# Kernel optimization log

Hardware: AMD Instinct MI355X
Metric: run time of the kernel (lower is better)

The kernel has to match this reference:

```python
import jax, jax.numpy as jnp
import numpy as np

D_MODEL = 1024
N_HEADS = 16
D_K = D_MODEL // N_HEADS
B, S = 4, 2048


def setup_inputs() -> dict:
    key = jax.random.key(0)
    ks = jax.random.split(key, 9)
    sc = 1.0 / np.sqrt(D_MODEL)
    inp = {
        "x": jax.random.normal(ks[0], (B, S, D_MODEL), dtype=jnp.float32),
        # causal mask, broadcastable over batch and heads; 0 -> masked
        "mask": jnp.tril(jnp.ones((S, S), dtype=jnp.int32))[None, None, :, :],
        "Wq": jax.random.normal(ks[1], (D_MODEL, D_MODEL), dtype=jnp.float32) * sc,
        "bq": jax.random.normal(ks[2], (D_MODEL,), dtype=jnp.float32) * sc,
        "Wk": jax.random.normal(ks[3], (D_MODEL, D_MODEL), dtype=jnp.float32) * sc,
        "bk": jax.random.normal(ks[4], (D_MODEL,), dtype=jnp.float32) * sc,
        "Wv": jax.random.normal(ks[5], (D_MODEL, D_MODEL), dtype=jnp.float32) * sc,
        "bv": jax.random.normal(ks[6], (D_MODEL,), dtype=jnp.float32) * sc,
        "Wo": jax.random.normal(ks[7], (D_MODEL, D_MODEL), dtype=jnp.float32) * sc,
        "bo": jax.random.normal(ks[8], (D_MODEL,), dtype=jnp.float32) * sc,
    }
    return inp


def _split_heads(t):
    b, s, _ = t.shape
    return t.reshape(b, s, N_HEADS, D_K).transpose(0, 2, 1, 3)  # [B,H,S,dk]


def reference(x, mask, Wq, bq, Wk, bk, Wv, bv, Wo, bo):
    Q = _split_heads(x @ Wq.T + bq)
    K = _split_heads(x @ Wk.T + bk)
    V = _split_heads(x @ Wv.T + bv)
    scores = jnp.einsum("bhqd,bhkd->bhqk", Q, K) / jnp.sqrt(jnp.float32(D_K))
    scores = jnp.where(mask == 0, jnp.float32(-1e9), scores)
    weights = jax.nn.softmax(scores, axis=-1)
    attn = jnp.einsum("bhqk,bhkd->bhqd", weights, V)  # [B,H,S,dk]
    attn = attn.transpose(0, 2, 1, 3).reshape(x.shape[0], x.shape[1], D_MODEL)
    return attn @ Wo.T + bo
```

## Files before the change

kernel.cpp:

```cpp
#include <hip/hip_runtime.h>
#include <hip/hip_bf16.h>
#include <cstdint>

#define DM   1024
#define NH   16
#define DK   64
#define BB   4
#define SS   2048
#define MTOT (BB * SS)
#define PAD  68

typedef short short8 __attribute__((ext_vector_type(8)));
typedef float f32x4  __attribute__((ext_vector_type(4)));
using u16 = unsigned short;

__device__ inline u16 f2b(float f) {
    union { float f; unsigned int u; } v; v.f = f;
    unsigned int u = v.u;
    u += 0x7fffu + ((u >> 16) & 1u);
    return (u16)(u >> 16);
}
__device__ inline u16 f2b_trunc(float f) {
    union { float f; unsigned int u; } v; v.f = f;
    return (u16)(v.u >> 16);
}
__device__ inline float b2f(u16 s) {
    union { unsigned int u; float f; } v; v.u = ((unsigned int)s) << 16;
    return v.f;
}

__device__ inline void load_lds16(const u16* g, u16* l) {
    __builtin_amdgcn_global_load_lds(
        (const __attribute__((address_space(1))) unsigned int*)g,
        (__attribute__((address_space(3))) unsigned int*)l, 16, 0, 0);
}

struct CvtPtrs {
    const void *x, *Wq, *Wk, *Wv, *Wo, *bq, *bk, *bv, *bo;
    u16 *xb, *Wqb, *Wkb, *Wvb, *Wob, *bqb, *bkb, *bvb, *bob;
};

__global__ void convert_all(CvtPtrs p, int* __restrict__ flag)
{
    __shared__ int cnt;
    if (threadIdx.x == 0) cnt = 0;
    __syncthreads();
    int c = 0;
    for (int i = threadIdx.x; i < 512; i += 256) {
        const int e = (((const u16*)p.x)[i] >> 7) & 0xFF;
        if (e >= 100 && e <= 140) c++;
    }
    atomicAdd(&cnt, c);
    __syncthreads();
    const int isbf = (cnt >= 420) ? 1 : 0;
    if (blockIdx.x == 0 && threadIdx.x == 0) *flag = isbf;
    if (isbf) return;

    const size_t E  = (size_t)MTOT * DM;
    const size_t W1 = (size_t)DM * DM;
    const size_t i = ((size_t)blockIdx.x * blockDim.x + threadIdx.x) * 8;
    const float* s; u16* d; size_t off;
    if (i < E) {
        s = (const float*)p.x; d = p.xb; off = i;
    } else {
        size_t j = i - E;
        if (j < (W1 << 2)) {
            const int w = (int)(j >> 20); off = j & (W1 - 1);
            const float* ss[4] = {(const float*)p.Wq, (const float*)p.Wk,
                                  (const float*)p.Wv, (const float*)p.Wo};
            u16* dd[4] = {p.Wqb, p.Wkb, p.Wvb, p.Wob};
            s = ss[w]; d = dd[w];
        } else {
            j -= (W1 << 2);
            if (j >= 4 * DM) return;
            const int w = (int)(j >> 10); off = j & (DM - 1);
            const float* ss[4] = {(const float*)p.bq, (const float*)p.bk,
                                  (const float*)p.bv, (const float*)p.bo};
            u16* dd[4] = {p.bqb, p.bkb, p.bvb, p.bob};
            s = ss[w]; d = dd[w];
        }
    }
    const float4 f0 = *(const float4*)(s + off);
    const float4 f1 = *(const float4*)(s + off + 4);
    u16 tmp[8] = {f2b(f0.x), f2b(f0.y), f2b(f0.z), f2b(f0.w),
                  f2b(f1.x), f2b(f1.y), f2b(f1.z), f2b(f1.w)};
    *(int4*)(d + off) = *(const int4*)tmp;
}

__device__ __forceinline__
void gemm_body(const u16* __restrict__ A, const u16* __restrict__ Bw,
               const u16* __restrict__ bias, void* __restrict__ out,
               int mode, float scale, int isbf, int m0, int n0,
               u16 (*As)[64], u16 (*Bs)[64])
{
    const int tid  = threadIdx.x;
    const int wave = tid >> 6;
    const int lane = tid & 63;
    const int wm = (wave >> 1) * 64;
    const int wn = (wave & 1) * 64;

    const int lm   = lane & 15;
    const int quad = lane >> 4;
    const int kq   = quad * 8;
    const int rq   = quad * 4;

    const int lrow   = lane >> 3;
    const int lchunk = (lane & 7) ^ lrow;
    const u16* gA = A  + (size_t)(m0 + 8*wave + lrow) * DM + lchunk * 8;
    const u16* gB = Bw + (size_t)(n0 + 8*wave + lrow) * DM + lchunk * 8;
    u16* ldsA = (u16*)((char*)&As[0][0] + wave * 1024);
    u16* ldsB = (u16*)((char*)&Bs[0][0] + wave * 1024);

    f32x4 acc[4][4] = {};

    for (int k0 = 0; k0 < DM; k0 += 64) {
        __syncthreads();
#pragma unroll
        for (int c = 0; c < 4; c++) {
            load_lds16(gA + (size_t)c*32*DM + k0, (u16*)((char*)ldsA + c*4096));
            load_lds16(gB + (size_t)c*32*DM + k0, (u16*)((char*)ldsB + c*4096));
        }
        __syncthreads();

#pragma unroll
        for (int ks = 0; ks < 2; ks++) {
            const int ca = ((ks*4 + quad) ^ (lm & 7)) * 8;
            short8 af[4], bf[4];
#pragma unroll
            for (int i = 0; i < 4; i++) af[i] = *(const short8*)(&As[wm + 16*i + lm][ca]);
#pragma unroll
            for (int j = 0; j < 4; j++) bf[j] = *(const short8*)(&Bs[wn + 16*j + lm][ca]);
#pragma unroll
            for (int i = 0; i < 4; i++)
#pragma unroll
                for (int j = 0; j < 4; j++)
                    acc[i][j] = __builtin_amdgcn_mfma_f32_16x16x32_bf16(af[i], bf[j], acc[i][j], 0, 0, 0);
        }
    }

#pragma unroll
    for (int j = 0; j < 4; j++) {
        const int col = n0 + wn + 16*j + lm;
        const float bv = b2f(bias[col]);
        const int h = col >> 6, d = col & 63;
#pragma unroll
        for (int i = 0; i < 4; i++) {
            if (mode == 2) {
                const int row0 = m0 + wm + 16*i + rq;
                const int b = row0 >> 11, s = row0 & 2047;
                u16 tmp[4];
#pragma unroll
                for (int r = 0; r < 4; r++)
                    tmp[r] = f2b((acc[i][j][r] + bv) * scale);
                const size_t idx = (((size_t)(b*NH + h) * DK) + d) * SS + s;
                *(uint2*)(&((u16*)out)[idx]) = *(const uint2*)tmp;
            } else {
#pragma unroll
                for (int r = 0; r < 4; r++) {
                    const int row = m0 + wm + 16*i + rq + r;
                    const float v = (acc[i][j][r] + bv) * scale;
                    if (mode == 0) {
                        const size_t idx = (size_t)row * DM + col;
                        if (isbf) ((u16*)out)[idx] = f2b(v);
                        else      ((float*)out)[idx] = v;
                    } else {
                        const int b = row >> 11, s = row & 2047;
                        const size_t idx = (((size_t)(b*NH + h) * SS) + s) * DK + d;
                        ((u16*)out)[idx] = f2b(v);
                    }
                }
            }
        }
    }
}

__global__ __launch_bounds__(256)
void gemm_qkv(CvtPtrs p, u16* __restrict__ Qb, u16* __restrict__ Kb,
              u16* __restrict__ Vb, float qscale, const int* __restrict__ flag)
{
    __shared__ __align__(16) u16 As[128][64];
    __shared__ __align__(16) u16 Bs[128][64];
    const int id  = blockIdx.x;
    const int xcd = id & 7;
    const int j   = id >> 3;
    const int m0  = (xcd * 8 + (j & 7)) * 128;
    const int n0  = ((j >> 3) & 7) * 128;
    const int z   = j >> 6;
    const int isbf = *flag;
    const u16* A = isbf ? (const u16*)p.x : p.xb;
    const u16* Bw, *bias; u16* out;
    if (z == 0)      { Bw = isbf ? (const u16*)p.Wq : p.Wqb; bias = isbf ? (const u16*)p.bq : p.bqb; out = Qb; }
    else if (z == 1) { Bw = isbf ? (const u16*)p.Wk : p.Wkb; bias = isbf ? (const u16*)p.bk : p.bkb; out = Kb; }
    else             { Bw = isbf ? (const u16*)p.Wv : p.Wvb; bias = isbf ? (const u16*)p.bv : p.bvb; out = Vb; }
    const int mode  = (z == 2) ? 2 : 1;
    const float sc  = (z == 0) ? qscale : 1.0f;
    gemm_body(A, Bw, bias, out, mode, sc, 1, m0, n0, As, Bs);
}

__global__ __launch_bounds__(256)
void gemm_out(const u16* __restrict__ Ab, CvtPtrs p, void* __restrict__ out,
              const int* __restrict__ flag)
{
    __shared__ __align__(16) u16 As[128][64];
    __shared__ __align__(16) u16 Bs[128][64];
    const int id  = blockIdx.x;
    const int xcd = id & 7;
    const int j   = id >> 3;
    const int m0  = (xcd * 8 + (j & 7)) * 128;
    const int n0  = (j >> 3) * 128;
    const int isbf = *flag;
    const u16* Bw   = isbf ? (const u16*)p.Wo : p.Wob;
    const u16* bias = isbf ? (const u16*)p.bo : p.bob;
    gemm_body(Ab, Bw, bias, out, 0, 1.0f, isbf, m0, n0, As, Bs);
}

__global__ __launch_bounds__(256)
void attn_causal(const u16* __restrict__ Q, const u16* __restrict__ K,
                 const u16* __restrict__ VT, u16* __restrict__ O)
{
    __shared__ __align__(16) u16 Ks[2][64][PAD];
    __shared__ __align__(16) u16 Vs[2][64][PAD];
    __shared__ __align__(16) u16 Ps[128][PAD];

    const int tid  = threadIdx.x;
    const int wave = tid >> 6;
    const int lane = tid & 63;
    const int qx = blockIdx.x;
    const int h = blockIdx.y, b = blockIdx.z;
    const int bh = b * NH + h;

    const u16* Kg = K  + (size_t)bh * SS * DK;
    const u16* Vg = VT + (size_t)bh * DK * SS;

    const int srow = tid >> 3;
    const int scol = (tid & 7) * 8;
    const int lm = lane & 15, quad = lane >> 4, kq = quad * 8, rq = quad * 4;

#pragma unroll
    for (int seg = 0; seg < 2; seg++) {
        const int qt = seg ? (15 - qx) : qx;
        const int q0 = qt * 128;
        const int nt = 2 * (qt + 1);
        const u16* Qg = Q + ((size_t)bh * SS + q0) * DK;

        short8 qa[2][2];
#pragma unroll
        for (int mi = 0; mi < 2; mi++)
#pragma unroll
            for (int ks = 0; ks < 2; ks++)
                qa[mi][ks] = *(const short8*)(&Qg[(size_t)(32*wave + 16*mi + lm) * DK + ks*32 + kq]);

        int4 kv0 = *(const int4*)(&Kg[(size_t)srow * DK + scol]);
        int4 kv1 = *(const int4*)(&Kg[(size_t)(srow + 32) * DK + scol]);
        int4 vv0 = *(const int4*)(&Vg[(size_t)srow * SS + scol]);
        int4 vv1 = *(const int4*)(&Vg[(size_t)(srow + 32) * SS + scol]);
        *(int4*)(&Ks[0][srow][scol])      = kv0;
        *(int4*)(&Ks[0][srow + 32][scol]) = kv1;
        *(int4*)(&Vs[0][srow][scol])      = vv0;
        *(int4*)(&Vs[0][srow + 32][scol]) = vv1;
        __syncthreads();

        kv0 = *(const int4*)(&Kg[(size_t)(64 + srow) * DK + scol]);
        kv1 = *(const int4*)(&Kg[(size_t)(64 + srow + 32) * DK + scol]);
        vv0 = *(const int4*)(&Vg[(size_t)srow * SS + 64 + scol]);
        vv1 = *(const int4*)(&Vg[(size_t)(srow + 32) * SS + 64 + scol]);

        f32x4 o[2][4] = {};
        float lacc[2][4] = {};

        for (int t = 0; t < nt; t++) {
            const int buf = t & 1;
            const int k0 = 64 * t;

            f32x4 sc[2][4] = {};
#pragma unroll
            for (int ks = 0; ks < 2; ks++)
#pragma unroll
                for (int j = 0; j < 4; j++) {
                    const short8 bfr = *(const short8*)(&Ks[buf][16*j + lm][ks*32 + kq]);
                    sc[0][j] = __builtin_amdgcn_mfma_f32_16x16x32_bf16(qa[0][ks], bfr, sc[0][j], 0, 0, 0);
                    sc[1][j] = __builtin_amdgcn_mfma_f32_16x16x32_bf16(qa[1][ks], bfr, sc[1][j], 0, 0, 0);
                }

            if (k0 + 63 > q0 + 32*wave) {
#pragma unroll
                for (int mi = 0; mi < 2; mi++)
#pragma unroll
                    for (int j = 0; j < 4; j++)
#pragma unroll
                        for (int r = 0; r < 4; r++)
                            if (k0 + 16*j + lm > q0 + 32*wave + 16*mi + rq + r)
                                sc[mi][j][r] = -1e30f;
            }

#pragma unroll
            for (int mi = 0; mi < 2; mi++)
#pragma unroll
                for (int j = 0; j < 4; j++)
#pragma unroll
                    for (int r = 0; r < 4; r++) {
                        const float pv = __builtin_amdgcn_exp2f(sc[mi][j][r]);
                        lacc[mi][r] += pv;
                        Ps[32*wave + 16*mi + rq + r][16*j + lm] = f2b_trunc(pv);
                    }

#pragma unroll
            for (int ks = 0; ks < 2; ks++) {
                const short8 pa0 = *(const short8*)(&Ps[32*wave + lm][ks*32 + kq]);
                const short8 pa1 = *(const short8*)(&Ps[32*wave + 16 + lm][ks*32 + kq]);
#pragma unroll
                for (int j = 0; j < 4; j++) {
                    const short8 vfr = *(const short8*)(&Vs[buf][16*j + lm][ks*32 + kq]);
                    o[0][j] = __builtin_amdgcn_mfma_f32_16x16x32_bf16(pa0, vfr, o[0][j], 0, 0, 0);
                    o[1][j] = __builtin_amdgcn_mfma_f32_16x16x32_bf16(pa1, vfr, o[1][j], 0, 0, 0);
                }
            }

            if (t + 1 < nt) {
                const int nb = buf ^ 1;
                *(int4*)(&Ks[nb][srow][scol])      = kv0;
                *(int4*)(&Ks[nb][srow + 32][scol]) = kv1;
                *(int4*)(&Vs[nb][srow][scol])      = vv0;
                *(int4*)(&Vs[nb][srow + 32][scol]) = vv1;
                if (t + 2 < nt) {
                    const int kn = 64 * (t + 2);
                    kv0 = *(const int4*)(&Kg[(size_t)(kn + srow) * DK + scol]);
                    kv1 = *(const int4*)(&Kg[(size_t)(kn + srow + 32) * DK + scol]);
                    vv0 = *(const int4*)(&Vg[(size_t)srow * SS + kn + scol]);
                    vv1 = *(const int4*)(&Vg[(size_t)(srow + 32) * SS + kn + scol]);
                }
            }
            __syncthreads();
        }

#pragma unroll
        for (int mi = 0; mi < 2; mi++)
#pragma unroll
            for (int r = 0; r < 4; r++) {
                float v = lacc[mi][r];
#pragma unroll
                for (int off = 1; off < 16; off <<= 1)
                    v += __shfl_xor(v, off, 64);
                const float inv = 1.f / v;
                const size_t rowg = (size_t)b * SS + q0 + 32*wave + 16*mi + rq + r;
#pragma unroll
                for (int j = 0; j < 4; j++)
                    O[rowg * DM + h*DK + 16*j + lm] = f2b(o[mi][j][r] * inv);
            }
    }
}

extern "C" void kernel_launch(void* const* d_in, const int* in_sizes, int n_in,
                              void* d_out, int out_size, void* d_ws, size_t ws_size,
                              hipStream_t stream)
{
    (void)in_sizes; (void)n_in; (void)out_size; (void)ws_size;

    int* flag = (int*)d_ws;
    u16* ws = (u16*)((char*)d_ws + 16);

    const size_t E  = (size_t)MTOT * DM;
    const size_t W1 = (size_t)DM * DM;
    u16* xb  = ws;
    u16* Wqb = ws + E;
    u16* Wkb = Wqb + W1;
    u16* Wvb = Wkb + W1;
    u16* Wob = Wvb + W1;
    u16* bqb = Wob + W1;
    u16* bkb = bqb + DM;
    u16* bvb = bkb + DM;
    u16* bob = bvb + DM;
    u16* Qb  = bob + DM;
    u16* Kb  = Qb + E;
    u16* Vb  = Kb + E;
    u16* Ab  = xb;

    CvtPtrs p;
    p.x = d_in[0];
    p.Wq = d_in[2]; p.bq = d_in[3];
    p.Wk = d_in[4]; p.bk = d_in[5];
    p.Wv = d_in[6]; p.bv = d_in[7];
    p.Wo = d_in[8]; p.bo = d_in[9];
    p.xb = xb;
    p.Wqb = Wqb; p.Wkb = Wkb; p.Wvb = Wvb; p.Wob = Wob;
    p.bqb = bqb; p.bkb = bkb; p.bvb = bvb; p.bob = bob;

    const int cvt_blocks = (int)((E + 4*W1 + 4*DM) / 2048);
    convert_all<<<cvt_blocks, 256, 0, stream>>>(p, flag);

    const float qscale = 0.18033688011112042f;

    gemm_qkv<<<1536, 256, 0, stream>>>(p, Qb, Kb, Vb, qscale, flag);
    attn_causal<<<dim3(SS/256, NH, BB), 256, 0, stream>>>(Qb, Kb, Vb, Ab);
    gemm_out<<<512, 256, 0, stream>>>(Ab, p, d_out, flag);
}
```

Baseline: 294.6 us.

## Use two-wave 64x128 warp tiles in QKV GEMM to raise fragment reuse

```diff
diff --git a/kernel.cpp b/kernel.cpp
--- a/kernel.cpp
+++ b/kernel.cpp
@@ -88,20 +88,17 @@
 }
 
 __device__ __forceinline__
-void gemm_body(const u16* __restrict__ A, const u16* __restrict__ Bw,
-               const u16* __restrict__ bias, void* __restrict__ out,
-               int mode, float scale, int isbf, int m0, int n0,
-               u16 (*As)[64], u16 (*Bs)[64])
+void gemm_body2(const u16* __restrict__ A, const u16* __restrict__ Bw,
+                const u16* __restrict__ bias, void* __restrict__ out,
+                int mode, float scale, int isbf, int m0, int n0,
+                u16 (*As)[64], u16 (*Bs)[64])
 {
     const int tid  = threadIdx.x;
     const int wave = tid >> 6;
     const int lane = tid & 63;
-    const int wm = (wave >> 1) * 64;
-    const int wn = (wave & 1) * 64;
 
     const int lm   = lane & 15;
     const int quad = lane >> 4;
-    const int kq   = quad * 8;
     const int rq   = quad * 4;
 
     const int lrow   = lane >> 3;
@@ -111,42 +108,42 @@
     u16* ldsA = (u16*)((char*)&As[0][0] + wave * 1024);
     u16* ldsB = (u16*)((char*)&Bs[0][0] + wave * 1024);
 
-    f32x4 acc[4][4] = {};
+    f32x4 acc[4][8] = {};
 
     for (int k0 = 0; k0 < DM; k0 += 64) {
         __syncthreads();
 #pragma unroll
-        for (int c = 0; c < 4; c++) {
-            load_lds16(gA + (size_t)c*32*DM + k0, (u16*)((char*)ldsA + c*4096));
-            load_lds16(gB + (size_t)c*32*DM + k0, (u16*)((char*)ldsB + c*4096));
+        for (int c = 0; c < 8; c++) {
+            load_lds16(gA + (size_t)c*16*DM + k0, (u16*)((char*)ldsA + c*2048));
+            load_lds16(gB + (size_t)c*16*DM + k0, (u16*)((char*)ldsB + c*2048));
         }
         __syncthreads();
 
 #pragma unroll
         for (int ks = 0; ks < 2; ks++) {
             const int ca = ((ks*4 + quad) ^ (lm & 7)) * 8;
-            short8 af[4], bf[4];
-#pragma unroll
-            for (int i = 0; i < 4; i++) af[i] = *(const short8*)(&As[wm + 16*i + lm][ca]);
-#pragma unroll
-            for (int j = 0; j < 4; j++) bf[j] = *(const short8*)(&Bs[wn + 16*j + lm][ca]);
+            short8 af[4], bf[8];
+#pragma unroll
+            for (int i = 0; i < 4; i++) af[i] = *(const short8*)(&As[64*wave + 16*i + lm][ca]);
+#pragma unroll
+            for (int j = 0; j < 8; j++) bf[j] = *(const short8*)(&Bs[16*j + lm][ca]);
 #pragma unroll
             for (int i = 0; i < 4; i++)
 #pragma unroll
-                for (int j = 0; j < 4; j++)
+                for (int j = 0; j < 8; j++)
                     acc[i][j] = __builtin_amdgcn_mfma_f32_16x16x32_bf16(af[i], bf[j], acc[i][j], 0, 0, 0);
         }
     }
 
 #pragma unroll
-    for (int j = 0; j < 4; j++) {
-        const int col = n0 + wn + 16*j + lm;
+    for (int j = 0; j < 8; j++) {
+        const int col = n0 + 16*j + lm;
         const float bv = b2f(bias[col]);
         const int h = col >> 6, d = col & 63;
 #pragma unroll
         for (int i = 0; i < 4; i++) {
             if (mode == 2) {
-                const int row0 = m0 + wm + 16*i + rq;
+                const int row0 = m0 + 64*wave + 16*i + rq;
                 const int b = row0 >> 11, s = row0 & 2047;
                 u16 tmp[4];
 #pragma unroll
@@ -157,7 +154,7 @@
             } else {
 #pragma unroll
                 for (int r = 0; r < 4; r++) {
-                    const int row = m0 + wm + 16*i + rq + r;
+                    const int row = m0 + 64*wave + 16*i + rq + r;
                     const float v = (acc[i][j][r] + bv) * scale;
                     if (mode == 0) {
                         const size_t idx = (size_t)row * DM + col;
@@ -174,7 +171,75 @@
     }
 }
 
-__global__ __launch_bounds__(256)
+__device__ __forceinline__
+void gemm_body4(const u16* __restrict__ A, const u16* __restrict__ Bw,
+                const u16* __restrict__ bias, void* __restrict__ out,
+                int mode, float scale, int isbf, int m0, int n0,
+                u16 (*As)[64], u16 (*Bs)[64])
+{
+    const int tid  = threadIdx.x;
+    const int wave = tid >> 6;
+    const int lane = tid & 63;
+    const int wm = (wave >> 1) * 64;
+    const int wn = (wave & 1) * 64;
+
+    const int lm   = lane & 15;
+    const int quad = lane >> 4;
+    const int rq   = quad * 4;
+
+    const int lrow   = lane >> 3;
+    const int lchunk = (lane & 7) ^ lrow;
+    const u16* gA = A  + (size_t)(m0 + 8*wave + lrow) * DM + lchunk * 8;
+    const u16* gB = Bw + (size_t)(n0 + 8*wave + lrow) * DM + lchunk * 8;
+    u16* ldsA = (u16*)((char*)&As[0][0] + wave * 1024);
+    u16* ldsB = (u16*)((char*)&Bs[0][0] + wave * 1024);
+
+    f32x4 acc[4][4] = {};
+
+    for (int k0 = 0; k0 < DM; k0 += 64) {
+        __syncthreads();
+#pragma unroll
+        for (int c = 0; c < 4; c++) {
+            load_lds16(gA + (size_t)c*32*DM + k0, (u16*)((char*)ldsA + c*4096));
+            load_lds16(gB + (size_t)c*32*DM + k0, (u16*)((char*)ldsB + c*4096));
+        }
+        __syncthreads();
+
+#pragma unroll
+        for (int ks = 0; ks < 2; ks++) {
+            const int ca = ((ks*4 + quad) ^ (lm & 7)) * 8;
+            short8 af[4], bf[4];
+#pragma unroll
+            for (int i = 0; i < 4; i++) af[i] = *(const short8*)(&As[wm + 16*i + lm][ca]);
+#pragma unroll
+            for (int j = 0; j < 4; j++) bf[j] = *(const short8*)(&Bs[wn + 16*j + lm][ca]);
+#pragma unroll
+            for (int i = 0; i < 4; i++)
+#pragma unroll
+                for (int j = 0; j < 4; j++)
+                    acc[i][j] = __builtin_amdgcn_mfma_f32_16x16x32_bf16(af[i], bf[j], acc[i][j], 0, 0, 0);
+        }
+    }
+
+#pragma unroll
+    for (int j = 0; j < 4; j++) {
+        const int col = n0 + wn + 16*j + lm;
+        const float bv = b2f(bias[col]);
+#pragma unroll
+        for (int i = 0; i < 4; i++) {
+#pragma unroll
+            for (int r = 0; r < 4; r++) {
+                const int row = m0 + wm + 16*i + rq + r;
+                const float v = (acc[i][j][r] + bv) * scale;
+                const size_t idx = (size_t)row * DM + col;
+                if (isbf) ((u16*)out)[idx] = f2b(v);
+                else      ((float*)out)[idx] = v;
+            }
+        }
+    }
+}
+
+__global__ __launch_bounds__(128, 2)
 void gemm_qkv(CvtPtrs p, u16* __restrict__ Qb, u16* __restrict__ Kb,
               u16* __restrict__ Vb, float qscale, const int* __restrict__ flag)
 {
@@ -194,7 +259,7 @@
     else             { Bw = isbf ? (const u16*)p.Wv : p.Wvb; bias = isbf ? (const u16*)p.bv : p.bvb; out = Vb; }
     const int mode  = (z == 2) ? 2 : 1;
     const float sc  = (z == 0) ? qscale : 1.0f;
-    gemm_body(A, Bw, bias, out, mode, sc, 1, m0, n0, As, Bs);
+    gemm_body2(A, Bw, bias, out, mode, sc, 1, m0, n0, As, Bs);
 }
 
 __global__ __launch_bounds__(256)
@@ -211,7 +276,7 @@
     const int isbf = *flag;
     const u16* Bw   = isbf ? (const u16*)p.Wo : p.Wob;
     const u16* bias = isbf ? (const u16*)p.bo : p.bob;
-    gemm_body(Ab, Bw, bias, out, 0, 1.0f, isbf, m0, n0, As, Bs);
+    gemm_body4(Ab, Bw, bias, out, 0, 1.0f, isbf, m0, n0, As, Bs);
 }
 
 __global__ __launch_bounds__(256)
@@ -390,7 +455,7 @@
 
     const float qscale = 0.18033688011112042f;
 
-    gemm_qkv<<<1536, 256, 0, stream>>>(p, Qb, Kb, Vb, qscale, flag);
+    gemm_qkv<<<1536, 128, 0, stream>>>(p, Qb, Kb, Vb, qscale, flag);
     attn_causal<<<dim3(SS/256, NH, BB), 256, 0, stream>>>(Qb, Kb, Vb, Ab);
     gemm_out<<<512, 256, 0, stream>>>(Ab, p, d_out, flag);
 }
```

Measured after the change: 298.7 us. About the same (+1.4%).

## Double-buffer GEMM LDS tiles with register-staged prefetch

Applied to the files above, without the earlier changes.

```diff
diff --git a/kernel.cpp b/kernel.cpp
--- a/kernel.cpp
+++ b/kernel.cpp
@@ -27,12 +27,6 @@
 __device__ inline float b2f(u16 s) {
     union { unsigned int u; float f; } v; v.u = ((unsigned int)s) << 16;
     return v.f;
-}
-
-__device__ inline void load_lds16(const u16* g, u16* l) {
-    __builtin_amdgcn_global_load_lds(
-        (const __attribute__((address_space(1))) unsigned int*)g,
-        (__attribute__((address_space(3))) unsigned int*)l, 16, 0, 0);
 }
 
 struct CvtPtrs {
@@ -88,10 +82,10 @@
 }
 
 __device__ __forceinline__
-void gemm_body(const u16* __restrict__ A, const u16* __restrict__ Bw,
-               const u16* __restrict__ bias, void* __restrict__ out,
-               int mode, float scale, int isbf, int m0, int n0,
-               u16 (*As)[64], u16 (*Bs)[64])
+void gemm_body_db(const u16* __restrict__ A, const u16* __restrict__ Bw,
+                  const u16* __restrict__ bias, void* __restrict__ out,
+                  int mode, float scale, int isbf, int m0, int n0,
+                  u16 (*As)[128][64], u16 (*Bs)[128][64])
 {
     const int tid  = threadIdx.x;
     const int wave = tid >> 6;
@@ -101,41 +95,69 @@
 
     const int lm   = lane & 15;
     const int quad = lane >> 4;
-    const int kq   = quad * 8;
     const int rq   = quad * 4;
 
-    const int lrow   = lane >> 3;
-    const int lchunk = (lane & 7) ^ lrow;
-    const u16* gA = A  + (size_t)(m0 + 8*wave + lrow) * DM + lchunk * 8;
-    const u16* gB = Bw + (size_t)(n0 + 8*wave + lrow) * DM + lchunk * 8;
-    u16* ldsA = (u16*)((char*)&As[0][0] + wave * 1024);
-    u16* ldsB = (u16*)((char*)&Bs[0][0] + wave * 1024);
+    const int srow = tid >> 1;
+    const int sc4  = (tid & 1) * 4;
+    const u16* gA = A  + (size_t)(m0 + srow) * DM + sc4 * 8;
+    const u16* gB = Bw + (size_t)(n0 + srow) * DM + sc4 * 8;
+    const int swz = srow & 7;
+
+    int4 ra[4], rb[4];
+#pragma unroll
+    for (int c = 0; c < 4; c++) {
+        ra[c] = *(const int4*)(gA + c*8);
+        rb[c] = *(const int4*)(gB + c*8);
+    }
+#pragma unroll
+    for (int c = 0; c < 4; c++) {
+        *(int4*)(&As[0][srow][((sc4 + c) ^ swz) * 8]) = ra[c];
+        *(int4*)(&Bs[0][srow][((sc4 + c) ^ swz) * 8]) = rb[c];
+    }
+#pragma unroll
+    for (int c = 0; c < 4; c++) {
+        ra[c] = *(const int4*)(gA + 64 + c*8);
+        rb[c] = *(const int4*)(gB + 64 + c*8);
+    }
+    __syncthreads();
 
     f32x4 acc[4][4] = {};
 
-    for (int k0 = 0; k0 < DM; k0 += 64) {
-        __syncthreads();
-#pragma unroll
-        for (int c = 0; c < 4; c++) {
-            load_lds16(gA + (size_t)c*32*DM + k0, (u16*)((char*)ldsA + c*4096));
-            load_lds16(gB + (size_t)c*32*DM + k0, (u16*)((char*)ldsB + c*4096));
-        }
-        __syncthreads();
+    for (int t = 0; t < 16; t++) {
+        const int buf = t & 1;
 
 #pragma unroll
         for (int ks = 0; ks < 2; ks++) {
             const int ca = ((ks*4 + quad) ^ (lm & 7)) * 8;
             short8 af[4], bf[4];
 #pragma unroll
-            for (int i = 0; i < 4; i++) af[i] = *(const short8*)(&As[wm + 16*i + lm][ca]);
-#pragma unroll
-            for (int j = 0; j < 4; j++) bf[j] = *(const short8*)(&Bs[wn + 16*j + lm][ca]);
+            for (int i = 0; i < 4; i++) af[i] = *(const short8*)(&As[buf][wm + 16*i + lm][ca]);
+#pragma unroll
+            for (int j = 0; j < 4; j++) bf[j] = *(const short8*)(&Bs[buf][wn + 16*j + lm][ca]);
 #pragma unroll
             for (int i = 0; i < 4; i++)
 #pragma unroll
                 for (int j = 0; j < 4; j++)
                     acc[i][j] = __builtin_amdgcn_mfma_f32_16x16x32_bf16(af[i], bf[j], acc[i][j], 0, 0, 0);
         }
+
+        if (t + 1 < 16) {
+            const int nb = buf ^ 1;
+#pragma unroll
+            for (int c = 0; c < 4; c++) {
+                *(int4*)(&As[nb][srow][((sc4 + c) ^ swz) * 8]) = ra[c];
+                *(int4*)(&Bs[nb][srow][((sc4 + c) ^ swz) * 8]) = rb[c];
+            }
+            if (t + 2 < 16) {
+                const int kn = (t + 2) * 64;
+#pragma unroll
+                for (int c = 0; c < 4; c++) {
+                    ra[c] = *(const int4*)(gA + kn + c*8);
+                    rb[c] = *(const int4*)(gB + kn + c*8);
+                }
+            }
+        }
+        __syncthreads();
     }
 
 #pragma unroll
@@ -178,8 +200,8 @@
 void gemm_qkv(CvtPtrs p, u16* __restrict__ Qb, u16* __restrict__ Kb,
               u16* __restrict__ Vb, float qscale, const int* __restrict__ flag)
 {
-    __shared__ __align__(16) u16 As[128][64];
-    __shared__ __align__(16) u16 Bs[128][64];
+    __shared__ __align__(16) u16 As[2][128][64];
+    __shared__ __align__(16) u16 Bs[2][128][64];
     const int id  = blockIdx.x;
     const int xcd = id & 7;
     const int j   = id >> 3;
@@ -194,15 +216,15 @@
     else             { Bw = isbf ? (const u16*)p.Wv : p.Wvb; bias = isbf ? (const u16*)p.bv : p.bvb; out = Vb; }
     const int mode  = (z == 2) ? 2 : 1;
     const float sc  = (z == 0) ? qscale : 1.0f;
-    gemm_body(A, Bw, bias, out, mode, sc, 1, m0, n0, As, Bs);
+    gemm_body_db(A, Bw, bias, out, mode, sc, 1, m0, n0, As, Bs);
 }
 
 __global__ __launch_bounds__(256)
 void gemm_out(const u16* __restrict__ Ab, CvtPtrs p, void* __restrict__ out,
               const int* __restrict__ flag)
 {
-    __shared__ __align__(16) u16 As[128][64];
-    __shared__ __align__(16) u16 Bs[128][64];
+    __shared__ __align__(16) u16 As[2][128][64];
+    __shared__ __align__(16) u16 Bs[2][128][64];
     const int id  = blockIdx.x;
     const int xcd = id & 7;
     const int j   = id >> 3;
@@ -211,7 +233,7 @@
     const int isbf = *flag;
     const u16* Bw   = isbf ? (const u16*)p.Wo : p.Wob;
     const u16* bias = isbf ? (const u16*)p.bo : p.bob;
-    gemm_body(Ab, Bw, bias, out, 0, 1.0f, isbf, m0, n0, As, Bs);
+    gemm_body_db(Ab, Bw, bias, out, 0, 1.0f, isbf, m0, n0, As, Bs);
 }
 
 __global__ __launch_bounds__(256)
```

Measured after the change: 448.4 us. 52.2% more time.

## Fuse fp32-to-bf16 conversion into GEMM tile loads, drop separate convert kernel

Applied to the files above, without the earlier changes.

```diff
diff --git a/kernel.cpp b/kernel.cpp
--- a/kernel.cpp
+++ b/kernel.cpp
@@ -35,62 +35,24 @@
         (__attribute__((address_space(3))) unsigned int*)l, 16, 0, 0);
 }
 
-struct CvtPtrs {
-    const void *x, *Wq, *Wk, *Wv, *Wo, *bq, *bk, *bv, *bo;
-    u16 *xb, *Wqb, *Wkb, *Wvb, *Wob, *bqb, *bkb, *bvb, *bob;
-};
-
-__global__ void convert_all(CvtPtrs p, int* __restrict__ flag)
-{
-    __shared__ int cnt;
-    if (threadIdx.x == 0) cnt = 0;
+__device__ inline int detect_bf16(const u16* x, int* cnt_sh)
+{
+    if (threadIdx.x == 0) *cnt_sh = 0;
     __syncthreads();
     int c = 0;
-    for (int i = threadIdx.x; i < 512; i += 256) {
-        const int e = (((const u16*)p.x)[i] >> 7) & 0xFF;
+    for (int i = threadIdx.x; i < 512; i += blockDim.x) {
+        const int e = (x[i] >> 7) & 0xFF;
         if (e >= 100 && e <= 140) c++;
     }
-    atomicAdd(&cnt, c);
+    atomicAdd(cnt_sh, c);
     __syncthreads();
-    const int isbf = (cnt >= 420) ? 1 : 0;
-    if (blockIdx.x == 0 && threadIdx.x == 0) *flag = isbf;
-    if (isbf) return;
-
-    const size_t E  = (size_t)MTOT * DM;
-    const size_t W1 = (size_t)DM * DM;
-    const size_t i = ((size_t)blockIdx.x * blockDim.x + threadIdx.x) * 8;
-    const float* s; u16* d; size_t off;
-    if (i < E) {
-        s = (const float*)p.x; d = p.xb; off = i;
-    } else {
-        size_t j = i - E;
-        if (j < (W1 << 2)) {
-            const int w = (int)(j >> 20); off = j & (W1 - 1);
-            const float* ss[4] = {(const float*)p.Wq, (const float*)p.Wk,
-                                  (const float*)p.Wv, (const float*)p.Wo};
-            u16* dd[4] = {p.Wqb, p.Wkb, p.Wvb, p.Wob};
-            s = ss[w]; d = dd[w];
-        } else {
-            j -= (W1 << 2);
-            if (j >= 4 * DM) return;
-            const int w = (int)(j >> 10); off = j & (DM - 1);
-            const float* ss[4] = {(const float*)p.bq, (const float*)p.bk,
-                                  (const float*)p.bv, (const float*)p.bo};
-            u16* dd[4] = {p.bqb, p.bkb, p.bvb, p.bob};
-            s = ss[w]; d = dd[w];
-        }
-    }
-    const float4 f0 = *(const float4*)(s + off);
-    const float4 f1 = *(const float4*)(s + off + 4);
-    u16 tmp[8] = {f2b(f0.x), f2b(f0.y), f2b(f0.z), f2b(f0.w),
-                  f2b(f1.x), f2b(f1.y), f2b(f1.z), f2b(f1.w)};
-    *(int4*)(d + off) = *(const int4*)tmp;
+    return (*cnt_sh >= 420) ? 1 : 0;
 }
 
 __device__ __forceinline__
-void gemm_body(const u16* __restrict__ A, const u16* __restrict__ Bw,
-               const u16* __restrict__ bias, void* __restrict__ out,
-               int mode, float scale, int isbf, int m0, int n0,
+void gemm_body(const void* __restrict__ A, const void* __restrict__ Bw,
+               const void* __restrict__ bias, void* __restrict__ out,
+               int mode, float scale, int abf, int isbf, int m0, int n0,
                u16 (*As)[64], u16 (*Bs)[64])
 {
     const int tid  = threadIdx.x;
@@ -101,13 +63,13 @@
 
     const int lm   = lane & 15;
     const int quad = lane >> 4;
-    const int kq   = quad * 8;
     const int rq   = quad * 4;
 
     const int lrow   = lane >> 3;
     const int lchunk = (lane & 7) ^ lrow;
-    const u16* gA = A  + (size_t)(m0 + 8*wave + lrow) * DM + lchunk * 8;
-    const u16* gB = Bw + (size_t)(n0 + 8*wave + lrow) * DM + lchunk * 8;
+
+    const u16* gA16 = (const u16*)A  + (size_t)(m0 + 8*wave + lrow) * DM + lchunk * 8;
+    const u16* gB16 = (const u16*)Bw + (size_t)(n0 + 8*wave + lrow) * DM + lchunk * 8;
     u16* ldsA = (u16*)((char*)&As[0][0] + wave * 1024);
     u16* ldsB = (u16*)((char*)&Bs[0][0] + wave * 1024);
 
@@ -115,10 +77,37 @@
 
     for (int k0 = 0; k0 < DM; k0 += 64) {
         __syncthreads();
-#pragma unroll
-        for (int c = 0; c < 4; c++) {
-            load_lds16(gA + (size_t)c*32*DM + k0, (u16*)((char*)ldsA + c*4096));
-            load_lds16(gB + (size_t)c*32*DM + k0, (u16*)((char*)ldsB + c*4096));
+        if (abf) {
+#pragma unroll
+            for (int c = 0; c < 4; c++)
+                load_lds16(gA16 + (size_t)c*32*DM + k0, (u16*)((char*)ldsA + c*4096));
+        } else {
+#pragma unroll
+            for (int c = 0; c < 4; c++) {
+                const int grow = c*32 + 8*wave + lrow;
+                const float* pa = (const float*)A + (size_t)(m0 + grow) * DM + k0 + lchunk * 8;
+                const float4 f0 = *(const float4*)pa;
+                const float4 f1 = *(const float4*)(pa + 4);
+                u16 tmp[8] = {f2b(f0.x), f2b(f0.y), f2b(f0.z), f2b(f0.w),
+                              f2b(f1.x), f2b(f1.y), f2b(f1.z), f2b(f1.w)};
+                *(int4*)(&As[grow][(lane & 7) * 8]) = *(const int4*)tmp;
+            }
+        }
+        if (isbf) {
+#pragma unroll
+            for (int c = 0; c < 4; c++)
+                load_lds16(gB16 + (size_t)c*32*DM + k0, (u16*)((char*)ldsB + c*4096));
+        } else {
+#pragma unroll
+            for (int c = 0; c < 4; c++) {
+                const int grow = c*32 + 8*wave + lrow;
+                const float* pb = (const float*)Bw + (size_t)(n0 + grow) * DM + k0 + lchunk * 8;
+                const float4 f0 = *(const float4*)pb;
+                const float4 f1 = *(const float4*)(pb + 4);
+                u16 tmp[8] = {f2b(f0.x), f2b(f0.y), f2b(f0.z), f2b(f0.w),
+                              f2b(f1.x), f2b(f1.y), f2b(f1.z), f2b(f1.w)};
+                *(int4*)(&Bs[grow][(lane & 7) * 8]) = *(const int4*)tmp;
+            }
         }
         __syncthreads();
 
@@ -141,7 +130,7 @@
 #pragma unroll
     for (int j = 0; j < 4; j++) {
         const int col = n0 + wn + 16*j + lm;
-        const float bv = b2f(bias[col]);
+        const float bv = isbf ? b2f(((const u16*)bias)[col]) : ((const float*)bias)[col];
         const int h = col >> 6, d = col & 63;
 #pragma unroll
         for (int i = 0; i < 4; i++) {
@@ -175,43 +164,50 @@
 }
 
 __global__ __launch_bounds__(256)
-void gemm_qkv(CvtPtrs p, u16* __restrict__ Qb, u16* __restrict__ Kb,
-              u16* __restrict__ Vb, float qscale, const int* __restrict__ flag)
+void gemm_qkv(const void* __restrict__ x,
+              const void* __restrict__ Wq, const void* __restrict__ Wk,
+              const void* __restrict__ Wv,
+              const void* __restrict__ bq, const void* __restrict__ bk,
+              const void* __restrict__ bv,
+              u16* __restrict__ Qb, u16* __restrict__ Kb, u16* __restrict__ Vb,
+              float qscale)
 {
     __shared__ __align__(16) u16 As[128][64];
     __shared__ __align__(16) u16 Bs[128][64];
+    __shared__ int cnt_sh;
+    const int isbf = detect_bf16((const u16*)x, &cnt_sh);
+
     const int id  = blockIdx.x;
     const int xcd = id & 7;
     const int j   = id >> 3;
     const int m0  = (xcd * 8 + (j & 7)) * 128;
     const int n0  = ((j >> 3) & 7) * 128;
     const int z   = j >> 6;
-    const int isbf = *flag;
-    const u16* A = isbf ? (const u16*)p.x : p.xb;
-    const u16* Bw, *bias; u16* out;
-    if (z == 0)      { Bw = isbf ? (const u16*)p.Wq : p.Wqb; bias = isbf ? (const u16*)p.bq : p.bqb; out = Qb; }
-    else if (z == 1) { Bw = isbf ? (const u16*)p.Wk : p.Wkb; bias = isbf ? (const u16*)p.bk : p.bkb; out = Kb; }
-    else             { Bw = isbf ? (const u16*)p.Wv : p.Wvb; bias = isbf ? (const u16*)p.bv : p.bvb; out = Vb; }
+    const void *Bw, *bias; u16* out;
+    if (z == 0)      { Bw = Wq; bias = bq; out = Qb; }
+    else if (z == 1) { Bw = Wk; bias = bk; out = Kb; }
+    else             { Bw = Wv; bias = bv; out = Vb; }
     const int mode  = (z == 2) ? 2 : 1;
     const float sc  = (z == 0) ? qscale : 1.0f;
-    gemm_body(A, Bw, bias, out, mode, sc, 1, m0, n0, As, Bs);
+    gemm_body(x, Bw, bias, out, mode, sc, isbf, isbf, m0, n0, As, Bs);
 }
 
 __global__ __launch_bounds__(256)
-void gemm_out(const u16* __restrict__ Ab, CvtPtrs p, void* __restrict__ out,
-              const int* __restrict__ flag)
+void gemm_out(const u16* __restrict__ Ab, const void* __restrict__ x,
+              const void* __restrict__ Wo, const void* __restrict__ bo,
+              void* __restrict__ out)
 {
     __shared__ __align__(16) u16 As[128][64];
     __shared__ __align__(16) u16 Bs[128][64];
+    __shared__ int cnt_sh;
+    const int isbf = detect_bf16((const u16*)x, &cnt_sh);
+
     const int id  = blockIdx.x;
     const int xcd = id & 7;
     const int j   = id >> 3;
     const int m0  = (xcd * 8 + (j & 7)) * 128;
     const int n0  = (j >> 3) * 128;
-    const int isbf = *flag;
-    const u16* Bw   = isbf ? (const u16*)p.Wo : p.Wob;
-    const u16* bias = isbf ? (const u16*)p.bo : p.bob;
-    gemm_body(Ab, Bw, bias, out, 0, 1.0f, isbf, m0, n0, As, Bs);
+    gemm_body(Ab, Wo, bo, out, 0, 1.0f, 1, isbf, m0, n0, As, Bs);
 }
 
 __global__ __launch_bounds__(256)
@@ -356,41 +352,27 @@
 {
     (void)in_sizes; (void)n_in; (void)out_size; (void)ws_size;
 
-    int* flag = (int*)d_ws;
-    u16* ws = (u16*)((char*)d_ws + 16);
-
-    const size_t E  = (size_t)MTOT * DM;
-    const size_t W1 = (size_t)DM * DM;
-    u16* xb  = ws;
-    u16* Wqb = ws + E;
-    u16* Wkb = Wqb + W1;
-    u16* Wvb = Wkb + W1;
-    u16* Wob = Wvb + W1;
-    u16* bqb = Wob + W1;
-    u16* bkb = bqb + DM;
-    u16* bvb = bkb + DM;
-    u16* bob = bvb + DM;
-    u16* Qb  = bob + DM;
-    u16* Kb  = Qb + E;
-    u16* Vb  = Kb + E;
-    u16* Ab  = xb;
-
-    CvtPtrs p;
-    p.x = d_in[0];
-    p.Wq = d_in[2]; p.bq = d_in[3];
-    p.Wk = d_in[4]; p.bk = d_in[5];
-    p.Wv = d_in[6]; p.bv = d_in[7];
-    p.Wo = d_in[8]; p.bo = d_in[9];
-    p.xb = xb;
-    p.Wqb = Wqb; p.Wkb = Wkb; p.Wvb = Wvb; p.Wob = Wob;
-    p.bqb = bqb; p.bkb = bkb; p.bvb = bvb; p.bob = bob;
-
-    const int cvt_blocks = (int)((E + 4*W1 + 4*DM) / 2048);
-    convert_all<<<cvt_blocks, 256, 0, stream>>>(p, flag);
+    const void* x  = d_in[0];
+    const void* Wq = d_in[2];
+    const void* bq = d_in[3];
+    const void* Wk = d_in[4];
+    const void* bk = d_in[5];
+    const void* Wv = d_in[6];
+    const void* bv = d_in[7];
+    const void* Wo = d_in[8];
+    const void* bo = d_in[9];
+
+    u16* ws = (u16*)d_ws;
+    const size_t E = (size_t)MTOT * DM;
+    u16* Qb = ws;
+    u16* Kb = ws + E;
+    u16* Vb = ws + 2*E;
+    u16* Ab = ws + 3*E;
 
     const float qscale = 0.18033688011112042f;
 
-    gemm_qkv<<<1536, 256, 0, stream>>>(p, Qb, Kb, Vb, qscale, flag);
+    gemm_qkv<<<1536, 256, 0, stream>>>(x, Wq, Wk, Wv, bq, bk, bv,
+                                       Qb, Kb, Vb, qscale);
     attn_causal<<<dim3(SS/256, NH, BB), 256, 0, stream>>>(Qb, Kb, Vb, Ab);
-    gemm_out<<<512, 256, 0, stream>>>(Ab, p, d_out, flag);
-}
+    gemm_out<<<512, 256, 0, stream>>>(Ab, x, Wo, bo, d_out);
+}
```

New measurement: 332.6 us. 12.9% more time.
